# Optimization experiments

Hardware: AMD Instinct MI355X
Metric: run time of the kernel (lower is better)

## Reference

```python
import jax, jax.numpy as jnp
import numpy as np

N_DATA = 200000   # num_data
DIM = 128         # input_dim
BATCH = 40000     # minibatch receptive-field nodes (rows of output, cols of subsampled_support)
E_SUB = 320000    # nnz of subsampled_support (avg sampled degree 8)
E_SUP = 1280000   # nnz of support rows for the batch (avg degree 32)


def setup_inputs() -> dict:
    key = jax.random.key(0)
    ks = jax.random.split(key, 9)
    inputs = jax.random.normal(ks[0], (BATCH, DIM), dtype=jnp.float32)
    # old cached activations (non-trainable variable, but a float tensor)
    old_activation = jax.random.normal(ks[1], (N_DATA, DIM), dtype=jnp.float32)
    input_fields = jax.random.randint(ks[2], (BATCH,), 0, N_DATA, dtype=jnp.int32)
    # subsampled_support: sparse [BATCH, BATCH] in COO
    sub_rows = jax.random.randint(ks[3], (E_SUB,), 0, BATCH, dtype=jnp.int32)
    sub_cols = jax.random.randint(ks[4], (E_SUB,), 0, BATCH, dtype=jnp.int32)
    sub_vals = jax.random.uniform(ks[5], (E_SUB,), dtype=jnp.float32)
    # support: sparse [BATCH, N_DATA] in COO
    sup_rows = jax.random.randint(ks[6], (E_SUP,), 0, BATCH, dtype=jnp.int32)
    sup_cols = jax.random.randint(ks[7], (E_SUP,), 0, N_DATA, dtype=jnp.int32)
    sup_vals = jax.random.uniform(ks[8], (E_SUP,), dtype=jnp.float32)
    return {
        "inputs": inputs,
        "old_activation": old_activation,
        "input_fields": input_fields,
        "sub_rows": sub_rows,
        "sub_cols": sub_cols,
        "sub_vals": sub_vals,
        "sup_rows": sup_rows,
        "sup_cols": sup_cols,
        "sup_vals": sup_vals,
    }


def _spmm(rows, cols, vals, dense, num_rows):
    # sparse [num_rows, K] (COO) @ dense [K, D] -> [num_rows, D]
    return jax.ops.segment_sum(vals[:, None] * dense[cols], rows, num_segments=num_rows)


def reference(inputs, old_activation, input_fields, sub_rows, sub_cols, sub_vals,
              sup_rows, sup_cols, sup_vals):
    M = inputs.shape[0]
    old = old_activation[input_fields]                      # [B, D] gather
    norm = lambda x: jnp.sqrt(jnp.sum(jnp.square(x)))
    sim = jnp.sum(inputs * old) / norm(inputs) / norm(old)  # logged scalar (tf.Print)
    diff = inputs - old
    out = _spmm(sub_rows, sub_cols, sub_vals, diff, M) \
        + _spmm(sup_rows, sup_cols, sup_vals, old_activation, M)
    return out, sim
```

## Files before the change

### kernel.cpp

```cpp
#include <hip/hip_runtime.h>
#include <math.h>

#define DIM 128
#define TPB 256
#define PREP_GRID 2048
#define SUB_CAP 32
#define SUP_CAP 64
#define OVER_MAX 65536
#define NXCD 8

__global__ void prep_bin_kernel(const float* __restrict__ inputs,
                                const float* __restrict__ old_act,
                                const int* __restrict__ fields,
                                const int* __restrict__ sub_rows, const int* __restrict__ sub_cols,
                                const float* __restrict__ sub_vals, int e_sub,
                                const int* __restrict__ sup_rows, const int* __restrict__ sup_cols,
                                const float* __restrict__ sup_vals, int e_sup,
                                int* __restrict__ cnt,
                                int2* __restrict__ pk_sub, int2* __restrict__ pk_sup,
                                int4* __restrict__ over,
                                float* __restrict__ partials, float* __restrict__ diff,
                                int use_diff, int nrows, int n4) {
    int tid = blockIdx.x * blockDim.x + threadIdx.x;
    int stride = gridDim.x * blockDim.x;
    int* over_cnt = cnt + 2 * nrows;

    float dot = 0.f, nx = 0.f, ny = 0.f;
    for (int i = tid; i < n4; i += stride) {
        int idx = i * 4;
        int b = idx >> 7, d = idx & (DIM - 1);
        float4 x = *(const float4*)(inputs + idx);
        int f = fields[b];
        float4 y = *(const float4*)(old_act + (size_t)f * DIM + d);
        dot += x.x * y.x + x.y * y.y + x.z * y.z + x.w * y.w;
        nx  += x.x * x.x + x.y * x.y + x.z * x.z + x.w * x.w;
        ny  += y.x * y.x + y.y * y.y + y.z * y.z + y.w * y.w;
        if (use_diff)
            *(float4*)(diff + idx) = make_float4(x.x - y.x, x.y - y.y, x.z - y.z, x.w - y.w);
    }

    int e_tot = e_sub + e_sup;
    int grp     = blockIdx.x & (NXCD - 1);
    int gblk    = blockIdx.x >> 3;
    int gtid    = gblk * blockDim.x + threadIdx.x;
    int gstride = (gridDim.x >> 3) * blockDim.x;
    for (int i = gtid; i < e_tot; i += gstride) {
        int r, sup, k;
        if (i < e_sub) { r = sub_rows[i]; sup = 0; k = i; }
        else           { k = i - e_sub; r = sup_rows[k]; sup = 1; }
        if ((r & (NXCD - 1)) != grp) continue;
        int c; float v;
        if (sup) { c = sup_cols[k]; v = sup_vals[k]; }
        else     { c = sub_cols[k]; v = sub_vals[k]; }
        int pos = atomicAdd(&cnt[sup ? nrows + r : r], 1);
        int cap = sup ? SUP_CAP : SUB_CAP;
        if (pos < cap) {
            int2* base = sup ? (pk_sup + (size_t)r * SUP_CAP) : (pk_sub + (size_t)r * SUB_CAP);
            base[pos] = make_int2(c, __float_as_int(v));
        } else {
            int op = atomicAdd(over_cnt, 1);
            if (op < OVER_MAX) over[op] = make_int4(r, c, __float_as_int(v), sup);
        }
    }

    for (int off = 32; off > 0; off >>= 1) {
        dot += __shfl_down(dot, off, 64);
        nx  += __shfl_down(nx,  off, 64);
        ny  += __shfl_down(ny,  off, 64);
    }
    __shared__ float s[3][4];
    int lane = threadIdx.x & 63, wv = threadIdx.x >> 6;
    if (lane == 0) { s[0][wv] = dot; s[1][wv] = nx; s[2][wv] = ny; }
    __syncthreads();
    if (threadIdx.x == 0) {
        float D = 0.f, NX = 0.f, NY = 0.f;
        for (int w = 0; w < 4; ++w) { D += s[0][w]; NX += s[1][w]; NY += s[2][w]; }
        partials[blockIdx.x * 3 + 0] = D;
        partials[blockIdx.x * 3 + 1] = NX;
        partials[blockIdx.x * 3 + 2] = NY;
    }
}

__global__ void row_bucket_kernel(const int* __restrict__ cnt,
                                  const int2* __restrict__ pk_sub, const int2* __restrict__ pk_sup,
                                  const float* __restrict__ diff,
                                  const float* __restrict__ inputs, const float* __restrict__ old_act,
                                  const int* __restrict__ fields,
                                  float* __restrict__ out, int nrows, int use_diff) {
    int wv = threadIdx.x >> 6, lane = threadIdx.x & 63;
    int r = blockIdx.x * (blockDim.x >> 6) + wv;
    if (r >= nrows) return;
    const int d0 = lane * 2;
    float a0 = 0.f, a1 = 0.f;

    {
        int e = cnt[r]; if (e > SUB_CAP) e = SUB_CAP;
        const int2* bp = pk_sub + (size_t)r * SUB_CAP;
        if (use_diff) {
            int j = 0;
            for (; j + 4 <= e; j += 4) {
                int4 qa = *(const int4*)(bp + j);
                int4 qb = *(const int4*)(bp + j + 2);
                float2 y0 = *(const float2*)(diff + (size_t)qa.x * DIM + d0);
                float2 y1 = *(const float2*)(diff + (size_t)qa.z * DIM + d0);
                float2 y2 = *(const float2*)(diff + (size_t)qb.x * DIM + d0);
                float2 y3 = *(const float2*)(diff + (size_t)qb.z * DIM + d0);
                a0 += __int_as_float(qa.y) * y0.x; a1 += __int_as_float(qa.y) * y0.y;
                a0 += __int_as_float(qa.w) * y1.x; a1 += __int_as_float(qa.w) * y1.y;
                a0 += __int_as_float(qb.y) * y2.x; a1 += __int_as_float(qb.y) * y2.y;
                a0 += __int_as_float(qb.w) * y3.x; a1 += __int_as_float(qb.w) * y3.y;
            }
            for (; j < e; ++j) {
                int2 p = bp[j];
                float2 y = *(const float2*)(diff + (size_t)p.x * DIM + d0);
                a0 += __int_as_float(p.y) * y.x;
                a1 += __int_as_float(p.y) * y.y;
            }
        } else {
            for (int j = 0; j < e; ++j) {
                int2 p = bp[j];
                int c = p.x; float v = __int_as_float(p.y);
                int f = fields[c];
                float2 x = *(const float2*)(inputs  + (size_t)c * DIM + d0);
                float2 y = *(const float2*)(old_act + (size_t)f * DIM + d0);
                a0 += v * (x.x - y.x);
                a1 += v * (x.y - y.y);
            }
        }
    }
    {
        int e = cnt[nrows + r]; if (e > SUP_CAP) e = SUP_CAP;
        const int2* bp = pk_sup + (size_t)r * SUP_CAP;
        int j = 0;
        for (; j + 8 <= e; j += 8) {
            int4 q0 = *(const int4*)(bp + j);
            int4 q1 = *(const int4*)(bp + j + 2);
            int4 q2 = *(const int4*)(bp + j + 4);
            int4 q3 = *(const int4*)(bp + j + 6);
            float2 y0 = *(const float2*)(old_act + (size_t)q0.x * DIM + d0);
            float2 y1 = *(const float2*)(old_act + (size_t)q0.z * DIM + d0);
            float2 y2 = *(const float2*)(old_act + (size_t)q1.x * DIM + d0);
            float2 y3 = *(const float2*)(old_act + (size_t)q1.z * DIM + d0);
            float2 y4 = *(const float2*)(old_act + (size_t)q2.x * DIM + d0);
            float2 y5 = *(const float2*)(old_act + (size_t)q2.z * DIM + d0);
            float2 y6 = *(const float2*)(old_act + (size_t)q3.x * DIM + d0);
            float2 y7 = *(const float2*)(old_act + (size_t)q3.z * DIM + d0);
            a0 += __int_as_float(q0.y) * y0.x; a1 += __int_as_float(q0.y) * y0.y;
            a0 += __int_as_float(q0.w) * y1.x; a1 += __int_as_float(q0.w) * y1.y;
            a0 += __int_as_float(q1.y) * y2.x; a1 += __int_as_float(q1.y) * y2.y;
            a0 += __int_as_float(q1.w) * y3.x; a1 += __int_as_float(q1.w) * y3.y;
            a0 += __int_as_float(q2.y) * y4.x; a1 += __int_as_float(q2.y) * y4.y;
            a0 += __int_as_float(q2.w) * y5.x; a1 += __int_as_float(q2.w) * y5.y;
            a0 += __int_as_float(q3.y) * y6.x; a1 += __int_as_float(q3.y) * y6.y;
            a0 += __int_as_float(q3.w) * y7.x; a1 += __int_as_float(q3.w) * y7.y;
        }
        for (; j < e; ++j) {
            int2 p = bp[j];
            float2 y = *(const float2*)(old_act + (size_t)p.x * DIM + d0);
            a0 += __int_as_float(p.y) * y.x;
            a1 += __int_as_float(p.y) * y.y;
        }
    }
    *(float2*)(out + (size_t)r * DIM + d0) = make_float2(a0, a1);
}

__global__ void tail_kernel(const float* __restrict__ partials, int np,
                            const int* __restrict__ cnt, const int4* __restrict__ over,
                            const float* __restrict__ diff,
                            const float* __restrict__ inputs, const float* __restrict__ old_act,
                            const int* __restrict__ fields,
                            float* __restrict__ out, int nrows, int n, int use_diff) {
    if (blockIdx.x == 0 && threadIdx.x < 64) {
        double dot = 0.0, nx = 0.0, ny = 0.0;
        for (int i = threadIdx.x; i < np; i += 64) {
            dot += (double)partials[i * 3 + 0];
            nx  += (double)partials[i * 3 + 1];
            ny  += (double)partials[i * 3 + 2];
        }
        for (int off = 32; off > 0; off >>= 1) {
            dot += __shfl_down(dot, off, 64);
            nx  += __shfl_down(nx,  off, 64);
            ny  += __shfl_down(ny,  off, 64);
        }
        if (threadIdx.x == 0)
            out[n] = (float)(dot / (sqrt(nx) * sqrt(ny)));
    }
    int no = cnt[2 * nrows]; if (no > OVER_MAX) no = OVER_MAX;
    int tid = blockIdx.x * blockDim.x + threadIdx.x;
    int stride = gridDim.x * blockDim.x;
    for (int i = tid; i < no; i += stride) {
        int4 t = over[i];
        int r = t.x, c = t.y, sup = t.w;
        float v = __int_as_float(t.z);
        for (int d = 0; d < DIM; ++d) {
            float term;
            if (sup) term = old_act[(size_t)c * DIM + d];
            else if (use_diff) term = diff[(size_t)c * DIM + d];
            else term = inputs[(size_t)c * DIM + d] - old_act[(size_t)fields[c] * DIM + d];
            atomicAdd(&out[(size_t)r * DIM + d], v * term);
        }
    }
}

__global__ void prep4_kernel(const float* __restrict__ inputs, const float* __restrict__ old_act,
                             const int* __restrict__ fields,
                             const int* __restrict__ sub_rows, int e_sub,
                             const int* __restrict__ sup_rows, int e_sup,
                             int* __restrict__ cnt, float* __restrict__ partials,
                             int nrows, int n2) {
    int tid = blockIdx.x * blockDim.x + threadIdx.x;
    int stride = gridDim.x * blockDim.x;
    float dot = 0.f, nx = 0.f, ny = 0.f;
    for (int i = tid; i < n2; i += stride) {
        int idx = i * 2;
        int b = idx >> 7, d = idx & (DIM - 1);
        float2 x = *(const float2*)(inputs + idx);
        int f = fields[b];
        float2 y = *(const float2*)(old_act + (size_t)f * DIM + d);
        dot += x.x * y.x + x.y * y.y;
        nx  += x.x * x.x + x.y * x.y;
        ny  += y.x * y.x + y.y * y.y;
    }
    int e_tot = e_sub + e_sup;
    for (int i = tid; i < e_tot; i += stride) {
        int r = (i < e_sub) ? sub_rows[i] : (nrows + sup_rows[i - e_sub]);
        atomicAdd(&cnt[r], 1);
    }
    for (int off = 32; off > 0; off >>= 1) {
        dot += __shfl_down(dot, off, 64);
        nx  += __shfl_down(nx,  off, 64);
        ny  += __shfl_down(ny,  off, 64);
    }
    __shared__ float s[3][4];
    int lane = threadIdx.x & 63, wv = threadIdx.x >> 6;
    if (lane == 0) { s[0][wv] = dot; s[1][wv] = nx; s[2][wv] = ny; }
    __syncthreads();
    if (threadIdx.x == 0) {
        float D = 0.f, NX = 0.f, NY = 0.f;
        for (int w = 0; w < 4; ++w) { D += s[0][w]; NX += s[1][w]; NY += s[2][w]; }
        partials[blockIdx.x * 3 + 0] = D;
        partials[blockIdx.x * 3 + 1] = NX;
        partials[blockIdx.x * 3 + 2] = NY;
    }
}

__global__ void finalize4_kernel(const float* __restrict__ partials, int np,
                                 float* __restrict__ out_sim) {
    double dot = 0.0, nx = 0.0, ny = 0.0;
    for (int i = threadIdx.x; i < np; i += 64) {
        dot += (double)partials[i * 3 + 0];
        nx  += (double)partials[i * 3 + 1];
        ny  += (double)partials[i * 3 + 2];
    }
    for (int off = 32; off > 0; off >>= 1) {
        dot += __shfl_down(dot, off, 64);
        nx  += __shfl_down(nx,  off, 64);
        ny  += __shfl_down(ny,  off, 64);
    }
    if (threadIdx.x == 0)
        *out_sim = (float)(dot / (sqrt(nx) * sqrt(ny)));
}

__global__ void scanA_kernel(const int* __restrict__ cnt, int* __restrict__ tmp,
                             int* __restrict__ bsum, int m) {
    __shared__ int s[256];
    int i = blockIdx.x * 256 + threadIdx.x;
    int v = (i < m) ? cnt[i] : 0;
    s[threadIdx.x] = v;
    __syncthreads();
    for (int d = 1; d < 256; d <<= 1) {
        int t = (threadIdx.x >= (unsigned)d) ? s[threadIdx.x - d] : 0;
        __syncthreads();
        s[threadIdx.x] += t;
        __syncthreads();
    }
    if (i < m) tmp[i] = s[threadIdx.x] - v;
    if (threadIdx.x == 255) bsum[blockIdx.x] = s[255];
}

__global__ void scanB_kernel(int* __restrict__ bsum, int* __restrict__ boff, int nb) {
    __shared__ int s[512];
    int v = (threadIdx.x < nb) ? bsum[threadIdx.x] : 0;
    s[threadIdx.x] = v;
    __syncthreads();
    for (int d = 1; d < 512; d <<= 1) {
        int t = (threadIdx.x >= (unsigned)d) ? s[threadIdx.x - d] : 0;
        __syncthreads();
        s[threadIdx.x] += t;
        __syncthreads();
    }
    if (threadIdx.x < nb) boff[threadIdx.x] = s[threadIdx.x] - v;
}

__global__ void scanC_kernel(const int* tmp, const int* __restrict__ boff,
                             int* __restrict__ off, int* cur, int m, int e_tot) {
    int i = blockIdx.x * 256 + threadIdx.x;
    if (i < m) {
        int o = tmp[i] + boff[i >> 8];
        off[i] = o;
        cur[i] = o;
    }
    if (i == 0) off[m] = e_tot;
}

__global__ void scatter4_kernel(const int* __restrict__ sub_rows, const int* __restrict__ sub_cols,
                                const float* __restrict__ sub_vals, int e_sub,
                                const int* __restrict__ sup_rows, const int* __restrict__ sup_cols,
                                const float* __restrict__ sup_vals, int e_sup,
                                int* __restrict__ cur, int2* __restrict__ pk, int nrows) {
    int i = blockIdx.x * blockDim.x + threadIdx.x;
    int e_tot = e_sub + e_sup;
    if (i >= e_tot) return;
    int r, c; float v;
    if (i < e_sub) { r = sub_rows[i]; c = sub_cols[i]; v = sub_vals[i]; }
    else { int k = i - e_sub; r = nrows + sup_rows[k]; c = sup_cols[k]; v = sup_vals[k]; }
    int pos = atomicAdd(&cur[r], 1);
    pk[pos] = make_int2(c, __float_as_int(v));
}

__global__ void row4_kernel(const int* __restrict__ off, const int2* __restrict__ pk,
                            const float* __restrict__ inputs, const float* __restrict__ old_act,
                            const int* __restrict__ fields, float* __restrict__ out, int nrows) {
    int wv = threadIdx.x >> 6, lane = threadIdx.x & 63;
    int r = blockIdx.x * (blockDim.x >> 6) + wv;
    if (r >= nrows) return;
    int d0 = lane * 2;
    float a0 = 0.f, a1 = 0.f;
    int b = off[r], e = off[r + 1];
    for (int j = b; j < e; ++j) {
        int2 p = pk[j];
        int c = p.x; float v = __int_as_float(p.y);
        int f = fields[c];
        float2 x = *(const float2*)(inputs  + (size_t)c * DIM + d0);
        float2 y = *(const float2*)(old_act + (size_t)f * DIM + d0);
        a0 += v * (x.x - y.x);
        a1 += v * (x.y - y.y);
    }
    b = off[nrows + r]; e = off[nrows + r + 1];
    for (int j = b; j < e; ++j) {
        int2 p = pk[j];
        int c = p.x; float v = __int_as_float(p.y);
        float2 y = *(const float2*)(old_act + (size_t)c * DIM + d0);
        a0 += v * y.x;
        a1 += v * y.y;
    }
    *(float2*)(out + (size_t)r * DIM + d0) = make_float2(a0, a1);
}

extern "C" void kernel_launch(void* const* d_in, const int* in_sizes, int n_in,
                              void* d_out, int out_size, void* d_ws, size_t ws_size,
                              hipStream_t stream) {
    const float* inputs   = (const float*)d_in[0];
    const float* old_act  = (const float*)d_in[1];
    const int*   fields   = (const int*)d_in[2];
    const int*   sub_rows = (const int*)d_in[3];
    const int*   sub_cols = (const int*)d_in[4];
    const float* sub_vals = (const float*)d_in[5];
    const int*   sup_rows = (const int*)d_in[6];
    const int*   sup_cols = (const int*)d_in[7];
    const float* sup_vals = (const float*)d_in[8];

    const int n     = in_sizes[0];
    const int nrows = n / DIM;
    const int e_sub = in_sizes[3];
    const int e_sup = in_sizes[6];
    const int e_tot = e_sub + e_sup;

    float* out = (float*)d_out;
    char*  ws  = (char*)d_ws;

    size_t off_part = 0;
    size_t off_cnt  = (PREP_GRID * 3 * 4 + 63) & ~(size_t)63;
    size_t off_over = (off_cnt + (size_t)(2 * nrows + 1) * 4 + 15) & ~(size_t)15;
    size_t off_psub = off_over + (size_t)OVER_MAX * 16;
    size_t off_psup = off_psub + (size_t)nrows * SUB_CAP * 8;
    size_t off_diff = off_psup + (size_t)nrows * SUP_CAP * 8;
    size_t need_base = off_diff;
    size_t need_diff = off_diff + (size_t)n * 4;

    if (ws_size >= need_base) {
        float* partials = (float*)(ws + off_part);
        int*   cnt      = (int*)(ws + off_cnt);
        int4*  over     = (int4*)(ws + off_over);
        int2*  pk_sub   = (int2*)(ws + off_psub);
        int2*  pk_sup   = (int2*)(ws + off_psup);
        float* diff     = (float*)(ws + off_diff);
        int use_diff    = (ws_size >= need_diff) ? 1 : 0;

        hipMemsetAsync(cnt, 0, (size_t)(2 * nrows + 1) * 4, stream);

        prep_bin_kernel<<<PREP_GRID, TPB, 0, stream>>>(
            inputs, old_act, fields,
            sub_rows, sub_cols, sub_vals, e_sub,
            sup_rows, sup_cols, sup_vals, e_sup,
            cnt, pk_sub, pk_sup, over, partials, diff, use_diff, nrows, n / 4);

        row_bucket_kernel<<<(nrows + 3) / 4, TPB, 0, stream>>>(
            cnt, pk_sub, pk_sup, diff, inputs, old_act, fields, out, nrows, use_diff);

        tail_kernel<<<32, TPB, 0, stream>>>(
            partials, PREP_GRID, cnt, over, diff, inputs, old_act, fields,
            out, nrows, n, use_diff);
        return;
    }

    const int m     = 2 * nrows;
    const int nblkA = (m + 255) / 256;
    size_t f_part = 0;
    size_t f_cnt  = (2048 * 3 * 4 + 63) & ~(size_t)63;
    size_t f_tmp  = f_cnt + (size_t)m * 4;
    size_t f_offs = f_tmp + (size_t)m * 4;
    size_t f_bsum = f_offs + (size_t)(m + 1) * 4;
    size_t f_boff = f_bsum + 4096;
    size_t f_pk   = (f_boff + 4096 + 7) & ~(size_t)7;
    size_t f_need = f_pk + (size_t)e_tot * 8;

    float* partials = (float*)(ws + f_part);
    int*   cnt      = (int*)(ws + f_cnt);
    int*   tmp      = (int*)(ws + f_tmp);
    int*   offs     = (int*)(ws + f_offs);
    int*   bsum     = (int*)(ws + f_bsum);
    int*   boff     = (int*)(ws + f_boff);
    int2*  pk       = (int2*)(ws + f_pk);

    if (ws_size >= f_need && nblkA <= 512) {
        hipMemsetAsync(cnt, 0, (size_t)m * 4, stream);
        prep4_kernel<<<2048, 256, 0, stream>>>(inputs, old_act, fields,
                                               sub_rows, e_sub, sup_rows, e_sup,
                                               cnt, partials, nrows, n / 2);
        scanA_kernel<<<nblkA, 256, 0, stream>>>(cnt, tmp, bsum, m);
        scanB_kernel<<<1, 512, 0, stream>>>(bsum, boff, nblkA);
        scanC_kernel<<<nblkA, 256, 0, stream>>>(tmp, boff, offs, tmp, m, e_tot);
        scatter4_kernel<<<(e_tot + 255) / 256, 256, 0, stream>>>(
            sub_rows, sub_cols, sub_vals, e_sub,
            sup_rows, sup_cols, sup_vals, e_sup, tmp, pk, nrows);
        row4_kernel<<<(nrows + 3) / 4, 256, 0, stream>>>(offs, pk, inputs, old_act,
                                                         fields, out, nrows);
        finalize4_kernel<<<1, 64, 0, stream>>>(partials, 2048, out + n);
    }
}
```

Measured before the change: 375.6 us.

## Split wavefront into half-waves gathering float4 rows with XCD-aware row mapping

```diff
diff --git a/kernel.cpp b/kernel.cpp
--- a/kernel.cpp
+++ b/kernel.cpp
@@ -88,43 +88,68 @@
                                   const int* __restrict__ fields,
                                   float* __restrict__ out, int nrows, int use_diff) {
     int wv = threadIdx.x >> 6, lane = threadIdx.x & 63;
-    int r = blockIdx.x * (blockDim.x >> 6) + wv;
+    int grp = blockIdx.x & (NXCD - 1);
+    int q   = blockIdx.x >> 3;
+    int r   = grp + NXCD * (q * 4 + wv);
     if (r >= nrows) return;
-    const int d0 = lane * 2;
-    float a0 = 0.f, a1 = 0.f;
+    const int half = lane >> 5;
+    const int l32  = lane & 31;
+    const int d4   = l32 * 4;
+    float a0 = 0.f, a1 = 0.f, a2 = 0.f, a3 = 0.f;
 
     {
         int e = cnt[r]; if (e > SUB_CAP) e = SUB_CAP;
         const int2* bp = pk_sub + (size_t)r * SUB_CAP;
+        int j = 0;
         if (use_diff) {
-            int j = 0;
-            for (; j + 4 <= e; j += 4) {
+            for (; j + 8 <= e; j += 8) {
                 int4 qa = *(const int4*)(bp + j);
                 int4 qb = *(const int4*)(bp + j + 2);
-                float2 y0 = *(const float2*)(diff + (size_t)qa.x * DIM + d0);
-                float2 y1 = *(const float2*)(diff + (size_t)qa.z * DIM + d0);
-                float2 y2 = *(const float2*)(diff + (size_t)qb.x * DIM + d0);
-                float2 y3 = *(const float2*)(diff + (size_t)qb.z * DIM + d0);
-                a0 += __int_as_float(qa.y) * y0.x; a1 += __int_as_float(qa.y) * y0.y;
-                a0 += __int_as_float(qa.w) * y1.x; a1 += __int_as_float(qa.w) * y1.y;
-                a0 += __int_as_float(qb.y) * y2.x; a1 += __int_as_float(qb.y) * y2.y;
-                a0 += __int_as_float(qb.w) * y3.x; a1 += __int_as_float(qb.w) * y3.y;
+                int4 qc = *(const int4*)(bp + j + 4);
+                int4 qd = *(const int4*)(bp + j + 6);
+                int   c0 = half ? qa.z : qa.x;  float v0 = __int_as_float(half ? qa.w : qa.y);
+                int   c1 = half ? qb.z : qb.x;  float v1 = __int_as_float(half ? qb.w : qb.y);
+                int   c2 = half ? qc.z : qc.x;  float v2 = __int_as_float(half ? qc.w : qc.y);
+                int   c3 = half ? qd.z : qd.x;  float v3 = __int_as_float(half ? qd.w : qd.y);
+                float4 g0 = *(const float4*)(diff + (size_t)c0 * DIM + d4);
+                float4 g1 = *(const float4*)(diff + (size_t)c1 * DIM + d4);
+                float4 g2 = *(const float4*)(diff + (size_t)c2 * DIM + d4);
+                float4 g3 = *(const float4*)(diff + (size_t)c3 * DIM + d4);
+                a0 += v0 * g0.x; a1 += v0 * g0.y; a2 += v0 * g0.z; a3 += v0 * g0.w;
+                a0 += v1 * g1.x; a1 += v1 * g1.y; a2 += v1 * g1.z; a3 += v1 * g1.w;
+                a0 += v2 * g2.x; a1 += v2 * g2.y; a2 += v2 * g2.z; a3 += v2 * g2.w;
+                a0 += v3 * g3.x; a1 += v3 * g3.y; a2 += v3 * g3.z; a3 += v3 * g3.w;
             }
-            for (; j < e; ++j) {
+            for (; j + 2 <= e; j += 2) {
+                int4 qa = *(const int4*)(bp + j);
+                int   c0 = half ? qa.z : qa.x;  float v0 = __int_as_float(half ? qa.w : qa.y);
+                float4 g0 = *(const float4*)(diff + (size_t)c0 * DIM + d4);
+                a0 += v0 * g0.x; a1 += v0 * g0.y; a2 += v0 * g0.z; a3 += v0 * g0.w;
+            }
+            if (j < e && half == 0) {
                 int2 p = bp[j];
-                float2 y = *(const float2*)(diff + (size_t)p.x * DIM + d0);
-                a0 += __int_as_float(p.y) * y.x;
-                a1 += __int_as_float(p.y) * y.y;
+                float v = __int_as_float(p.y);
+                float4 g = *(const float4*)(diff + (size_t)p.x * DIM + d4);
+                a0 += v * g.x; a1 += v * g.y; a2 += v * g.z; a3 += v * g.w;
             }
         } else {
-            for (int j = 0; j < e; ++j) {
+            for (; j + 2 <= e; j += 2) {
+                int4 qa = *(const int4*)(bp + j);
+                int   c0 = half ? qa.z : qa.x;  float v0 = __int_as_float(half ? qa.w : qa.y);
+                int   f0 = fields[c0];
+                float4 x0 = *(const float4*)(inputs  + (size_t)c0 * DIM + d4);
+                float4 y0 = *(const float4*)(old_act + (size_t)f0 * DIM + d4);
+                a0 += v0 * (x0.x - y0.x); a1 += v0 * (x0.y - y0.y);
+                a2 += v0 * (x0.z - y0.z); a3 += v0 * (x0.w - y0.w);
+            }
+            if (j < e && half == 0) {
                 int2 p = bp[j];
-                int c = p.x; float v = __int_as_float(p.y);
-                int f = fields[c];
-                float2 x = *(const float2*)(inputs  + (size_t)c * DIM + d0);
-                float2 y = *(const float2*)(old_act + (size_t)f * DIM + d0);
-                a0 += v * (x.x - y.x);
-                a1 += v * (x.y - y.y);
+                float v = __int_as_float(p.y);
+                int f = fields[p.x];
+                float4 x = *(const float4*)(inputs  + (size_t)p.x * DIM + d4);
+                float4 y = *(const float4*)(old_act + (size_t)f   * DIM + d4);
+                a0 += v * (x.x - y.x); a1 += v * (x.y - y.y);
+                a2 += v * (x.z - y.z); a3 += v * (x.w - y.w);
             }
         }
     }
@@ -132,36 +157,61 @@
         int e = cnt[nrows + r]; if (e > SUP_CAP) e = SUP_CAP;
         const int2* bp = pk_sup + (size_t)r * SUP_CAP;
         int j = 0;
-        for (; j + 8 <= e; j += 8) {
+        for (; j + 16 <= e; j += 16) {
             int4 q0 = *(const int4*)(bp + j);
             int4 q1 = *(const int4*)(bp + j + 2);
             int4 q2 = *(const int4*)(bp + j + 4);
             int4 q3 = *(const int4*)(bp + j + 6);
-            float2 y0 = *(const float2*)(old_act + (size_t)q0.x * DIM + d0);
-            float2 y1 = *(const float2*)(old_act + (size_t)q0.z * DIM + d0);
-            float2 y2 = *(const float2*)(old_act + (size_t)q1.x * DIM + d0);
-            float2 y3 = *(const float2*)(old_act + (size_t)q1.z * DIM + d0);
-            float2 y4 = *(const float2*)(old_act + (size_t)q2.x * DIM + d0);
-            float2 y5 = *(const float2*)(old_act + (size_t)q2.z * DIM + d0);
-            float2 y6 = *(const float2*)(old_act + (size_t)q3.x * DIM + d0);
-            float2 y7 = *(const float2*)(old_act + (size_t)q3.z * DIM + d0);
-            a0 += __int_as_float(q0.y) * y0.x; a1 += __int_as_float(q0.y) * y0.y;
-            a0 += __int_as_float(q0.w) * y1.x; a1 += __int_as_float(q0.w) * y1.y;
-            a0 += __int_as_float(q1.y) * y2.x; a1 += __int_as_float(q1.y) * y2.y;
-            a0 += __int_as_float(q1.w) * y3.x; a1 += __int_as_float(q1.w) * y3.y;
-            a0 += __int_as_float(q2.y) * y4.x; a1 += __int_as_float(q2.y) * y4.y;
-            a0 += __int_as_float(q2.w) * y5.x; a1 += __int_as_float(q2.w) * y5.y;
-            a0 += __int_as_float(q3.y) * y6.x; a1 += __int_as_float(q3.y) * y6.y;
-            a0 += __int_as_float(q3.w) * y7.x; a1 += __int_as_float(q3.w) * y7.y;
-        }
-        for (; j < e; ++j) {
+            int4 q4 = *(const int4*)(bp + j + 8);
+            int4 q5 = *(const int4*)(bp + j + 10);
+            int4 q6 = *(const int4*)(bp + j + 12);
+            int4 q7 = *(const int4*)(bp + j + 14);
+            int   c0 = half ? q0.z : q0.x;  float v0 = __int_as_float(half ? q0.w : q0.y);
+            int   c1 = half ? q1.z : q1.x;  float v1 = __int_as_float(half ? q1.w : q1.y);
+            int   c2 = half ? q2.z : q2.x;  float v2 = __int_as_float(half ? q2.w : q2.y);
+            int   c3 = half ? q3.z : q3.x;  float v3 = __int_as_float(half ? q3.w : q3.y);
+            int   c4 = half ? q4.z : q4.x;  float v4 = __int_as_float(half ? q4.w : q4.y);
+            int   c5 = half ? q5.z : q5.x;  float v5 = __int_as_float(half ? q5.w : q5.y);
+            int   c6 = half ? q6.z : q6.x;  float v6 = __int_as_float(half ? q6.w : q6.y);
+            int   c7 = half ? q7.z : q7.x;  float v7 = __int_as_float(half ? q7.w : q7.y);
+            float4 g0 = *(const float4*)(old_act + (size_t)c0 * DIM + d4);
+            float4 g1 = *(const float4*)(old_act + (size_t)c1 * DIM + d4);
+            float4 g2 = *(const float4*)(old_act + (size_t)c2 * DIM + d4);
+            float4 g3 = *(const float4*)(old_act + (size_t)c3 * DIM + d4);
+            float4 g4 = *(const float4*)(old_act + (size_t)c4 * DIM + d4);
+            float4 g5 = *(const float4*)(old_act + (size_t)c5 * DIM + d4);
+            float4 g6 = *(const float4*)(old_act + (size_t)c6 * DIM + d4);
+            float4 g7 = *(const float4*)(old_act + (size_t)c7 * DIM + d4);
+            a0 += v0 * g0.x; a1 += v0 * g0.y; a2 += v0 * g0.z; a3 += v0 * g0.w;
+            a0 += v1 * g1.x; a1 += v1 * g1.y; a2 += v1 * g1.z; a3 += v1 * g1.w;
+            a0 += v2 * g2.x; a1 += v2 * g2.y; a2 += v2 * g2.z; a3 += v2 * g2.w;
+            a0 += v3 * g3.x; a1 += v3 * g3.y; a2 += v3 * g3.z; a3 += v3 * g3.w;
+            a0 += v4 * g4.x; a1 += v4 * g4.y; a2 += v4 * g4.z; a3 += v4 * g4.w;
+            a0 += v5 * g5.x; a1 += v5 * g5.y; a2 += v5 * g5.z; a3 += v5 * g5.w;
+            a0 += v6 * g6.x; a1 += v6 * g6.y; a2 += v6 * g6.z; a3 += v6 * g6.w;
+            a0 += v7 * g7.x; a1 += v7 * g7.y; a2 += v7 * g7.z; a3 += v7 * g7.w;
+        }
+        for (; j + 2 <= e; j += 2) {
+            int4 qa = *(const int4*)(bp + j);
+            int   c0 = half ? qa.z : qa.x;  float v0 = __int_as_float(half ? qa.w : qa.y);
+            float4 g0 = *(const float4*)(old_act + (size_t)c0 * DIM + d4);
+            a0 += v0 * g0.x; a1 += v0 * g0.y; a2 += v0 * g0.z; a3 += v0 * g0.w;
+        }
+        if (j < e && half == 0) {
             int2 p = bp[j];
-            float2 y = *(const float2*)(old_act + (size_t)p.x * DIM + d0);
-            a0 += __int_as_float(p.y) * y.x;
-            a1 += __int_as_float(p.y) * y.y;
-        }
-    }
-    *(float2*)(out + (size_t)r * DIM + d0) = make_float2(a0, a1);
+            float v = __int_as_float(p.y);
+            float4 g = *(const float4*)(old_act + (size_t)p.x * DIM + d4);
+            a0 += v * g.x; a1 += v * g.y; a2 += v * g.z; a3 += v * g.w;
+        }
+    }
+    float b0 = __shfl(a0, lane ^ 32, 64);
+    float b1 = __shfl(a1, lane ^ 32, 64);
+    float b2 = __shfl(a2, lane ^ 32, 64);
+    float b3 = __shfl(a3, lane ^ 32, 64);
+    if (half == 0) {
+        float4 res = make_float4(a0 + b0, a1 + b1, a2 + b2, a3 + b3);
+        *(float4*)(out + (size_t)r * DIM + d4) = res;
+    }
 }
 
 __global__ void tail_kernel(const float* __restrict__ partials, int np,
@@ -395,7 +445,8 @@
             sup_rows, sup_cols, sup_vals, e_sup,
             cnt, pk_sub, pk_sup, over, partials, diff, use_diff, nrows, n / 4);
 
-        row_bucket_kernel<<<(nrows + 3) / 4, TPB, 0, stream>>>(
+        int nblk = NXCD * ((((nrows + NXCD - 1) / NXCD) + 3) / 4);
+        row_bucket_kernel<<<nblk, TPB, 0, stream>>>(
             cnt, pk_sub, pk_sup, diff, inputs, old_act, fields, out, nrows, use_diff);
 
         tail_kernel<<<32, TPB, 0, stream>>>(
```

Result: no change. 369.0 us (-1.8%).
